# Kernel optimization log

Measured on AMD Instinct MI355X. Metric: run time of the kernel, lower is better.

## Reference

```python
import jax, jax.numpy as jnp
import numpy as np

B, T, D, H, C = 256, 512, 128, 512, 10

def setup_inputs() -> dict:
    key = jax.random.key(0)
    ks = jax.random.split(key, 16)
    def kn(k, shape):  # kaiming-normal-ish init (gain irrelevant for correctness)
        fan_in = shape[-1]
        return jax.random.normal(k, shape, dtype=jnp.float32) * (1.0 / np.sqrt(fan_in))
    return {
        "x": jax.random.randint(ks[0], (B, T), 0, 3),
        "emb": jax.random.normal(ks[1], (3, D), dtype=jnp.float32),
        "Wfx": kn(ks[2], (H, D)), "Wfh": kn(ks[3], (H, H)), "bf": jnp.zeros((H,), jnp.float32),
        "Wix": kn(ks[4], (H, D)), "Wih": kn(ks[5], (H, H)), "bi": jnp.zeros((H,), jnp.float32),
        "Wox": kn(ks[6], (H, D)), "Woh": kn(ks[7], (H, H)), "bo": jnp.zeros((H,), jnp.float32),
        "Wcx": kn(ks[8], (H, D)), "bc": jnp.zeros((H,), jnp.float32),
        "Wph": kn(ks[9], (C, H)), "bp": jnp.zeros((C,), jnp.float32),
    }

def _forward(x, emb, Wfx, Wfh, bf, Wix, Wih, bi, Wox, Woh, bo, Wcx, bc, Wph, bp):
    xe = emb[x]  # [B, T, D]
    # Precompute input-to-gate projections as one big batched matmul each.
    fx = jnp.einsum('btd,hd->bth', xe, Wfx) + bf  # [B, T, H]
    ix = jnp.einsum('btd,hd->bth', xe, Wix) + bi
    ox = jnp.einsum('btd,hd->bth', xe, Wox) + bo
    cx = jnp.einsum('btd,hd->bth', xe, Wcx) + bc
    gates = jnp.stack([fx, ix, ox, cx], axis=0).transpose(2, 1, 0, 3)  # [T, B, 4, H]

    def step(carry, g):
        c, _ = carry
        gf, gi, go, gc = g[:, 0], g[:, 1], g[:, 2], g[:, 3]  # each [B, H]
        f = jax.nn.sigmoid(gf + c @ Wfh.T)
        i = jax.nn.sigmoid(gi + c @ Wih.T)
        o = jax.nn.sigmoid(go + c @ Woh.T)
        c_new = jax.nn.sigmoid(gc) * i + c * f
        h = jnp.tanh(c_new) * o
        return (c_new, h), None

    c0 = jnp.zeros((x.shape[0], Wfh.shape[0]), jnp.float32)
    (c_fin, h_fin), _ = jax.lax.scan(step, (c0, c0), gates)
    p = h_fin @ Wph.T + bp
    return jax.nn.log_softmax(p, axis=1)

def reference(x, emb, Wfx, Wfh, bf, Wix, Wih, bi, Wox, Woh, bo, Wcx, bc, Wph, bp):
    return _forward(x, emb, Wfx, Wfh, bf, Wix, Wih, bi, Wox, Woh, bo, Wcx, bc, Wph, bp)
```

## Files before the change

kernel.cpp:

```cpp
#include <hip/hip_runtime.h>
#include <stdint.h>

#define TLEN 512
#define HDIM 512
#define DDIM 128
#define NCLS 10

typedef float f32x4 __attribute__((ext_vector_type(4)));
typedef short bf16x8 __attribute__((ext_vector_type(8)));
typedef unsigned long long u64;

__device__ __forceinline__ unsigned short f2bf(float f) {
  union { float f; unsigned u; } v; v.f = f;
  return (unsigned short)((v.u + 0x7FFFu + ((v.u >> 16) & 1u)) >> 16);
}
__device__ __forceinline__ float bf2f(unsigned short h) {
  union { unsigned u; float f; } v; v.u = ((unsigned)h) << 16; return v.f;
}
__device__ __forceinline__ float sigm(float x) {
  return __builtin_amdgcn_rcpf(1.0f + __expf(-x));
}
__device__ __forceinline__ u64 ald(const u64* p) {
  return __hip_atomic_load(p, __ATOMIC_RELAXED, __HIP_MEMORY_SCOPE_AGENT);
}
__device__ __forceinline__ void ast16(unsigned short* p, unsigned short v) {
  __hip_atomic_store(p, v, __ATOMIC_RELAXED, __HIP_MEMORY_SCOPE_AGENT);
}
__device__ __forceinline__ void astd(unsigned* p, unsigned v) {
  __hip_atomic_store(p, v, __ATOMIC_RELAXED, __HIP_MEMORY_SCOPE_AGENT);
}

__global__ void k_gates(const float* __restrict__ emb,
                        const float* __restrict__ Wfx, const float* __restrict__ bf_,
                        const float* __restrict__ Wix, const float* __restrict__ bi_,
                        const float* __restrict__ Wcx, const float* __restrict__ bc_,
                        const float* __restrict__ Wox, const float* __restrict__ bo_,
                        float* __restrict__ G) {
  int tid = blockIdx.x * 256 + threadIdx.x;
  int h = tid & (HDIM - 1);
  int v = (tid >> 9) % 3;
  int g = tid / (3 * HDIM);
  const float* W; const float* bb;
  if (g == 0)      { W = Wfx; bb = bf_; }
  else if (g == 1) { W = Wix; bb = bi_; }
  else if (g == 2) { W = Wcx; bb = bc_; }
  else             { W = Wox; bb = bo_; }
  const float* e = emb + v * DDIM;
  const float* w = W + h * DDIM;
  float s = bb[h];
  #pragma unroll 8
  for (int d = 0; d < DDIM; ++d) s += e[d] * w[d];
  if (g == 2) s = sigm(s);
  G[tid] = s;
}

__global__ void k_pack_fi(const float* __restrict__ Wfh, const float* __restrict__ Wih,
                          unsigned short* __restrict__ pk) {
  int tid = blockIdx.x * 256 + threadIdx.x;
  int l  = tid & 63;
  int kt = (tid >> 6) & 15;
  int g  = (tid >> 10) & 1;
  int nt = (tid >> 11) & 3;
  int hs = (tid >> 13) & 7;
  int n  = hs * 64 + nt * 16 + (l & 15);
  int k0 = kt * 32 + (l >> 4) * 8;
  const float* src = (g ? Wih : Wfh) + n * HDIM + k0;
  unsigned short* dst = pk + (size_t)tid * 8;
  #pragma unroll
  for (int e = 0; e < 8; ++e) dst[e] = f2bf(src[e]);
}

__global__ void k_pack_o(const float* __restrict__ Woh, unsigned short* __restrict__ pk) {
  int tid = blockIdx.x * 256 + threadIdx.x;
  int l  = tid & 63;
  int kt = (tid >> 6) & 15;
  int nt = (tid >> 10) & 3;
  int hs = (tid >> 12) & 7;
  int n  = hs * 64 + nt * 16 + (l & 15);
  int k0 = kt * 32 + (l >> 4) * 8;
  const float* src = Woh + n * HDIM + k0;
  unsigned short* dst = pk + (size_t)tid * 8;
  #pragma unroll
  for (int e = 0; e < 8; ++e) dst[e] = f2bf(src[e]);
}

__global__ __launch_bounds__(256, 1)
void k_scan(const int* __restrict__ x, const float* __restrict__ G,
            const unsigned short* __restrict__ pk2,
            const unsigned short* __restrict__ pko,
            char* __restrict__ cbuf, unsigned* __restrict__ flg,
            unsigned short* __restrict__ hfin) {
  __shared__ float gts[12][68];
  __shared__ unsigned char xv[16][516];
  __shared__ uint4 lds_a[16][64];

  const int tid  = threadIdx.x;
  const int lane = tid & 63;
  const int w    = tid >> 6;
  const int bt   = blockIdx.x & 15;
  const int hs   = blockIdx.x >> 4;

  for (int j = tid; j < 12 * 64; j += 256) {
    int gv = j >> 6, c = j & 63;
    gts[gv][c] = G[gv * HDIM + hs * 64 + c];
  }
  for (int j = tid; j < 16 * TLEN; j += 256) {
    int r = j >> 9, tt = j & (TLEN - 1);
    xv[r][tt] = (unsigned char)x[(bt * 16 + r) * TLEN + tt];
  }

  bf16x8 wf[16], wi[16];
  {
    const bf16x8* ws = (const bf16x8*)pk2 + (size_t)((hs * 4 + w) * 2) * (16 * 64) + lane;
    #pragma unroll
    for (int kt = 0; kt < 16; ++kt) { wf[kt] = ws[kt * 64]; wi[kt] = ws[(16 + kt) * 64]; }
  }

  bf16x8 afr[16];
  #pragma unroll
  for (int kt = 0; kt < 16; ++kt) afr[kt] = bf16x8{0,0,0,0,0,0,0,0};

  float cf[4] = {0.f, 0.f, 0.f, 0.f};
  const int rgrp = (lane >> 4) * 4;
  const int coll = lane & 15;
  const int col  = w * 16 + coll;
  const int colb = (hs * 64 + col) * 2;
  const int rowb = (lane & 15) * 1024 + (lane >> 4) * 16;
  const f32x4 zz = {0.f, 0.f, 0.f, 0.f};

  __syncthreads();

  for (int t = 0; t < TLEN - 1; ++t) {
    f32x4 af = zz, ai = zz;
    #pragma unroll
    for (int kt = 0; kt < 16; ++kt) {
      af = __builtin_amdgcn_mfma_f32_16x16x32_bf16(afr[kt], wf[kt], af, 0, 0, 0);
      ai = __builtin_amdgcn_mfma_f32_16x16x32_bf16(afr[kt], wi[kt], ai, 0, 0, 0);
    }
    const unsigned tg = (unsigned)(t + 1);
    const int par = (int)(tg & 1);
    char* dbase = cbuf + par * 262144 + bt * 16384;

    #pragma unroll
    for (int r = 0; r < 4; ++r) {
      int vv = xv[rgrp + r][t];
      float fg = sigm(af[r] + gts[0 + vv][col]);
      float ig = sigm(ai[r] + gts[3 + vv][col]);
      float sc = gts[6 + vv][col];
      float cn = sc * ig + cf[r] * fg;
      cf[r] = cn;
      ast16((unsigned short*)(dbase + (rgrp + r) * 1024 + colb), f2bf(cn));
    }
    __syncthreads();

    unsigned* fl = flg + (par * 16 + bt) * 16;
    if (tid == 0) astd(fl + hs, tg);

    const u64 pat2 = ((u64)tg << 32) | (u64)tg;
    const u64* fp = (const u64*)fl;
    u64 g0, g1, g2, g3;
    do {
      g0 = ald(fp + 0); g1 = ald(fp + 1); g2 = ald(fp + 2); g3 = ald(fp + 3);
    } while (((g0 ^ pat2) | (g1 ^ pat2) | (g2 ^ pat2) | (g3 ^ pat2)) != 0ULL);
    asm volatile("" ::: "memory");

    const char* rb = dbase + rowb;
    #pragma unroll
    for (int i = 0; i < 4; ++i) {
      const int kt = (w << 2) | i;
      const u64* p = (const u64*)(rb + kt * 64);
      u64 lo = ald(p + 0), hi = ald(p + 1);
      uint4 q;
      q.x = (unsigned)lo; q.y = (unsigned)(lo >> 32);
      q.z = (unsigned)hi; q.w = (unsigned)(hi >> 32);
      lds_a[kt][lane] = q;
    }
    __syncthreads();
    #pragma unroll
    for (int kt = 0; kt < 16; ++kt) {
      union { uint4 q; bf16x8 v; } u;
      u.q = lds_a[kt][lane];
      afr[kt] = u.v;
    }
  }

  {
    const int t = TLEN - 1;
    bf16x8 wo[16];
    const bf16x8* os = (const bf16x8*)pko + (size_t)(hs * 4 + w) * (16 * 64) + lane;
    #pragma unroll
    for (int kt = 0; kt < 16; ++kt) wo[kt] = os[kt * 64];
    f32x4 af = zz, ai = zz, ao = zz;
    #pragma unroll
    for (int kt = 0; kt < 16; ++kt) {
      af = __builtin_amdgcn_mfma_f32_16x16x32_bf16(afr[kt], wf[kt], af, 0, 0, 0);
      ai = __builtin_amdgcn_mfma_f32_16x16x32_bf16(afr[kt], wi[kt], ai, 0, 0, 0);
      ao = __builtin_amdgcn_mfma_f32_16x16x32_bf16(afr[kt], wo[kt], ao, 0, 0, 0);
    }
    #pragma unroll
    for (int r = 0; r < 4; ++r) {
      int vv = xv[rgrp + r][t];
      float fg = sigm(af[r] + gts[0 + vv][col]);
      float ig = sigm(ai[r] + gts[3 + vv][col]);
      float sc = gts[6 + vv][col];
      float cn = sc * ig + cf[r] * fg;
      float og = sigm(ao[r] + gts[9 + vv][col]);
      float hv = tanhf(cn) * og;
      hfin[(bt * 16 + rgrp + r) * HDIM + hs * 64 + col] = f2bf(hv);
    }
  }
}

__global__ __launch_bounds__(64)
void k_head(const unsigned short* __restrict__ hfin, const float* __restrict__ Wph,
            const float* __restrict__ bp, float* __restrict__ out) {
  const int b = blockIdx.x;
  const int lane = threadIdx.x;
  float acc[NCLS];
  #pragma unroll
  for (int c = 0; c < NCLS; ++c) acc[c] = 0.f;
  const unsigned short* hrow = hfin + (size_t)b * HDIM;
  for (int k = lane; k < HDIM; k += 64) {
    float hv = bf2f(hrow[k]);
    #pragma unroll
    for (int c = 0; c < NCLS; ++c) acc[c] += hv * Wph[c * HDIM + k];
  }
  #pragma unroll
  for (int c = 0; c < NCLS; ++c)
    #pragma unroll
    for (int off = 32; off > 0; off >>= 1)
      acc[c] += __shfl_down(acc[c], off, 64);
  if (lane == 0) {
    float p[NCLS]; float m = -1e30f;
    #pragma unroll
    for (int c = 0; c < NCLS; ++c) { p[c] = acc[c] + bp[c]; m = fmaxf(m, p[c]); }
    float s = 0.f;
    #pragma unroll
    for (int c = 0; c < NCLS; ++c) s += __expf(p[c] - m);
    const float ls = __logf(s);
    #pragma unroll
    for (int c = 0; c < NCLS; ++c) out[b * NCLS + c] = p[c] - m - ls;
  }
}

extern "C" void kernel_launch(void* const* d_in, const int* in_sizes, int n_in,
                              void* d_out, int out_size, void* d_ws, size_t ws_size,
                              hipStream_t stream) {
  const int*   x   = (const int*)d_in[0];
  const float* emb = (const float*)d_in[1];
  const float* Wfx = (const float*)d_in[2];
  const float* Wfh = (const float*)d_in[3];
  const float* bf_ = (const float*)d_in[4];
  const float* Wix = (const float*)d_in[5];
  const float* Wih = (const float*)d_in[6];
  const float* bi_ = (const float*)d_in[7];
  const float* Wox = (const float*)d_in[8];
  const float* Woh = (const float*)d_in[9];
  const float* bo_ = (const float*)d_in[10];
  const float* Wcx = (const float*)d_in[11];
  const float* bc_ = (const float*)d_in[12];
  const float* Wph = (const float*)d_in[13];
  const float* bp_ = (const float*)d_in[14];

  char* ws = (char*)d_ws;
  float*          G    = (float*)(ws);
  unsigned short* hfin = (unsigned short*)(ws + 32768);
  char*           cbuf = (char*)(ws + 524288);
  unsigned*       flg  = (unsigned*)(ws + 1048576);
  unsigned short* pk2  = (unsigned short*)(ws + 1114112);
  unsigned short* pko  = (unsigned short*)(ws + 2162688);

  hipMemsetAsync(flg, 0, 2048, stream);
  hipLaunchKernelGGL(k_gates,   dim3(24),  dim3(256), 0, stream,
                     emb, Wfx, bf_, Wix, bi_, Wcx, bc_, Wox, bo_, G);
  hipLaunchKernelGGL(k_pack_fi, dim3(256), dim3(256), 0, stream, Wfh, Wih, pk2);
  hipLaunchKernelGGL(k_pack_o,  dim3(128), dim3(256), 0, stream, Woh, pko);
  hipLaunchKernelGGL(k_scan,    dim3(128), dim3(256), 0, stream, x, G, pk2, pko, cbuf, flg, hfin);
  hipLaunchKernelGGL(k_head,    dim3(256), dim3(64),  0, stream, hfin, Wph, bp_, (float*)d_out);
}
```

Measured before the change: 1.469 ms.

## Pad per-block flags to separate lines and use sc1 vector loads for exchange

Each block's step flag now sits in its own 64-byte slot. A wave polls the 8 flags of its group with one lane per flag and __all, instead of every thread reading four packed 64-bit words. The exchange of cell state between blocks now uses inline-asm global_load_dwordx4 with sc1 in place of paired 64-bit atomic loads, and the final-step Woh weight load is deferred until after the f/i MFMAs to reduce register pressure. The intent is to cut contention on the inter-block barrier and the latency of the per-step exchange. It depends on sc1 loads seeing other CUs' stores in time, which is a coherence risk.

```diff
diff --git a/kernel.cpp b/kernel.cpp
--- a/kernel.cpp
+++ b/kernel.cpp
@@ -8,7 +8,6 @@
 
 typedef float f32x4 __attribute__((ext_vector_type(4)));
 typedef short bf16x8 __attribute__((ext_vector_type(8)));
-typedef unsigned long long u64;
 
 __device__ __forceinline__ unsigned short f2bf(float f) {
   union { float f; unsigned u; } v; v.f = f;
@@ -20,15 +19,20 @@
 __device__ __forceinline__ float sigm(float x) {
   return __builtin_amdgcn_rcpf(1.0f + __expf(-x));
 }
-__device__ __forceinline__ u64 ald(const u64* p) {
-  return __hip_atomic_load(p, __ATOMIC_RELAXED, __HIP_MEMORY_SCOPE_AGENT);
-}
 __device__ __forceinline__ void ast16(unsigned short* p, unsigned short v) {
   __hip_atomic_store(p, v, __ATOMIC_RELAXED, __HIP_MEMORY_SCOPE_AGENT);
 }
 __device__ __forceinline__ void astd(unsigned* p, unsigned v) {
   __hip_atomic_store(p, v, __ATOMIC_RELAXED, __HIP_MEMORY_SCOPE_AGENT);
 }
+__device__ __forceinline__ unsigned aldd(const unsigned* p) {
+  return __hip_atomic_load(p, __ATOMIC_RELAXED, __HIP_MEMORY_SCOPE_AGENT);
+}
+
+#define GLOAD_SC1(dst, addr) \
+  asm volatile("global_load_dwordx4 %0, %1, off sc1" : "=&v"(dst) : "v"(addr))
+#define VMWAIT() do { asm volatile("s_waitcnt vmcnt(0)" ::: "memory"); \
+                      __builtin_amdgcn_sched_barrier(0); } while (0)
 
 __global__ void k_gates(const float* __restrict__ emb,
                         const float* __restrict__ Wfx, const float* __restrict__ bf_,
@@ -100,12 +104,12 @@
   const int bt   = blockIdx.x & 15;
   const int hs   = blockIdx.x >> 4;
 
-  for (int j = tid; j < 12 * 64; j += 256) {
-    int gv = j >> 6, c = j & 63;
+  for (int jj = tid; jj < 12 * 64; jj += 256) {
+    int gv = jj >> 6, c = jj & 63;
     gts[gv][c] = G[gv * HDIM + hs * 64 + c];
   }
-  for (int j = tid; j < 16 * TLEN; j += 256) {
-    int r = j >> 9, tt = j & (TLEN - 1);
+  for (int jj = tid; jj < 16 * TLEN; jj += 256) {
+    int r = jj >> 9, tt = jj & (TLEN - 1);
     xv[r][tt] = (unsigned char)x[(bt * 16 + r) * TLEN + tt];
   }
 
@@ -153,28 +157,24 @@
     }
     __syncthreads();
 
-    unsigned* fl = flg + (par * 16 + bt) * 16;
-    if (tid == 0) astd(fl + hs, tg);
-
-    const u64 pat2 = ((u64)tg << 32) | (u64)tg;
-    const u64* fp = (const u64*)fl;
-    u64 g0, g1, g2, g3;
-    do {
-      g0 = ald(fp + 0); g1 = ald(fp + 1); g2 = ald(fp + 2); g3 = ald(fp + 3);
-    } while (((g0 ^ pat2) | (g1 ^ pat2) | (g2 ^ pat2) | (g3 ^ pat2)) != 0ULL);
-    asm volatile("" ::: "memory");
-
-    const char* rb = dbase + rowb;
-    #pragma unroll
-    for (int i = 0; i < 4; ++i) {
-      const int kt = (w << 2) | i;
-      const u64* p = (const u64*)(rb + kt * 64);
-      u64 lo = ald(p + 0), hi = ald(p + 1);
-      uint4 q;
-      q.x = (unsigned)lo; q.y = (unsigned)(lo >> 32);
-      q.z = (unsigned)hi; q.w = (unsigned)(hi >> 32);
-      lds_a[kt][lane] = q;
-    }
+    unsigned* fl = flg + ((par * 16 + bt) * 8) * 16;
+    if (tid == 0) astd(fl + hs * 16, tg);
+
+    {
+      const unsigned* myf = fl + (lane & 7) * 16;
+      unsigned fv;
+      do { fv = aldd(myf); } while (!__all(fv == tg));
+    }
+
+    const char* rb = dbase + rowb + (w << 8);
+    uint4 q0, q1, q2, q3;
+    GLOAD_SC1(q0, rb);       GLOAD_SC1(q1, rb + 64);
+    GLOAD_SC1(q2, rb + 128); GLOAD_SC1(q3, rb + 192);
+    VMWAIT();
+    lds_a[(w << 2) | 0][lane] = q0;
+    lds_a[(w << 2) | 1][lane] = q1;
+    lds_a[(w << 2) | 2][lane] = q2;
+    lds_a[(w << 2) | 3][lane] = q3;
     __syncthreads();
     #pragma unroll
     for (int kt = 0; kt < 16; ++kt) {
@@ -186,17 +186,19 @@
 
   {
     const int t = TLEN - 1;
-    bf16x8 wo[16];
-    const bf16x8* os = (const bf16x8*)pko + (size_t)(hs * 4 + w) * (16 * 64) + lane;
-    #pragma unroll
-    for (int kt = 0; kt < 16; ++kt) wo[kt] = os[kt * 64];
     f32x4 af = zz, ai = zz, ao = zz;
     #pragma unroll
     for (int kt = 0; kt < 16; ++kt) {
       af = __builtin_amdgcn_mfma_f32_16x16x32_bf16(afr[kt], wf[kt], af, 0, 0, 0);
       ai = __builtin_amdgcn_mfma_f32_16x16x32_bf16(afr[kt], wi[kt], ai, 0, 0, 0);
+    }
+    bf16x8 wo[16];
+    const bf16x8* os = (const bf16x8*)pko + (size_t)(hs * 4 + w) * (16 * 64) + lane;
+    #pragma unroll
+    for (int kt = 0; kt < 16; ++kt) wo[kt] = os[kt * 64];
+    #pragma unroll
+    for (int kt = 0; kt < 16; ++kt)
       ao = __builtin_amdgcn_mfma_f32_16x16x32_bf16(afr[kt], wo[kt], ao, 0, 0, 0);
-    }
     #pragma unroll
     for (int r = 0; r < 4; ++r) {
       int vv = xv[rgrp + r][t];
@@ -265,16 +267,17 @@
   char* ws = (char*)d_ws;
   float*          G    = (float*)(ws);
   unsigned short* hfin = (unsigned short*)(ws + 32768);
+  unsigned*       flg  = (unsigned*)(ws + 294912);
   char*           cbuf = (char*)(ws + 524288);
-  unsigned*       flg  = (unsigned*)(ws + 1048576);
-  unsigned short* pk2  = (unsigned short*)(ws + 1114112);
-  unsigned short* pko  = (unsigned short*)(ws + 2162688);
-
-  hipMemsetAsync(flg, 0, 2048, stream);
+  unsigned short* pk2  = (unsigned short*)(ws + 1572864);
+  unsigned short* pko  = (unsigned short*)(ws + 2621440);
+
+  hipMemsetAsync(flg, 0, 16384, stream);
   hipLaunchKernelGGL(k_gates,   dim3(24),  dim3(256), 0, stream,
                      emb, Wfx, bf_, Wix, bi_, Wcx, bc_, Wox, bo_, G);
   hipLaunchKernelGGL(k_pack_fi, dim3(256), dim3(256), 0, stream, Wfh, Wih, pk2);
   hipLaunchKernelGGL(k_pack_o,  dim3(128), dim3(256), 0, stream, Woh, pko);
-  hipLaunchKernelGGL(k_scan,    dim3(128), dim3(256), 0, stream, x, G, pk2, pko, cbuf, flg, hfin);
+  hipLaunchKernelGGL(k_scan,    dim3(128), dim3(256), 0, stream,
+                     x, G, pk2, pko, cbuf, flg, hfin);
   hipLaunchKernelGGL(k_head,    dim3(256), dim3(64),  0, stream, hfin, Wph, bp_, (float*)d_out);
 }
```

New measurement: 1.260 ms. 14.2% less time.
